# Performance work log

Hardware: AMD Instinct MI355X
Metric: run time of the kernel (lower is better)

## Reference

```python
import jax, jax.numpy as jnp
import numpy as np

NUM_CLASSES = 20   # M = len(unique(true)); label 0 is background (skipped)
ALPHA = 0.7
BETA = 1.5


def setup_inputs() -> dict:
    key = jax.random.key(0)
    k1, k2, k3 = jax.random.split(key, 3)
    B, N, K = 1, 262144, 128
    points = jax.random.normal(k1, (B, N, 3), dtype=jnp.float32)
    true = jax.random.randint(k2, (B, N), 0, NUM_CLASSES)
    embedding = jax.random.normal(k3, (B, N, K), dtype=jnp.float32)
    return {"points": points, "true": true, "embedding": embedding}


def reference(points, true, embedding):
    # points: (B,N,3), true: (B,N) int labels in [0,M), embedding: (B,N,K). B == 1.
    B, N, K = embedding.shape
    M = NUM_CLASSES
    t = true[0]  # (N,)

    # g = sigmoid(||p||) per point
    g = jax.nn.sigmoid(jnp.sqrt(jnp.sum(points ** 2, axis=-1)))  # (B,N)

    # per-cluster counts and embedding means (segment reduce over N)
    counts = jax.ops.segment_sum(jnp.ones((N,), points.dtype), t, num_segments=M)  # (M,)
    safe_counts = jnp.maximum(counts, 1.0)
    means = jax.ops.segment_sum(embedding[0], t, num_segments=M) / safe_counts[:, None]  # (M,K)

    # intra-cluster: per point, distance to its cluster mean
    d = jnp.sqrt(jnp.sum((embedding - means[true]) ** 2, axis=-1))  # (B,N)
    per_point = g * jnp.square(jnp.maximum(d - ALPHA, 0.0))         # (B,N)
    intra_per_cluster = jax.ops.segment_sum(per_point[0], t, num_segments=M) / safe_counts  # (M,)
    intra = jnp.sum(intra_per_cluster[1:])  # sum over clusters 1..M-1 (skip background 0)

    # inter-cluster: pairwise mean distances among foreground clusters
    me = means[1:]                                    # (M-1, K)
    sq = jnp.sum((me[:, None, :] - me[None, :, :]) ** 2, axis=-1)  # (M-1, M-1)
    eye = jnp.eye(M - 1, dtype=sq.dtype)
    dist = jnp.sqrt(jnp.where(eye > 0, 1.0, sq))      # safe sqrt on diagonal
    inter = jnp.sum((1.0 - eye) * jnp.square(jnp.maximum(BETA - dist, 0.0)))

    return jnp.broadcast_to(intra / M + inter / (M * (M - 1)), (B,))
```

## Files before the change

### kernel.cpp

```cpp
#include <hip/hip_runtime.h>
#include <hip/hip_bf16.h>
#include <math.h>

#define NCLS 20
#define KDIM 128
#define ALPHA 0.7f
#define BETA 1.5f

#define WS_SUMS 0
#define WS_INTRA 2560
#define WS_CUR 2580
#define WS_ZERO_N 2600
#define WS_G 4096

#define GRID 2048
#define SUMS_GRID 1027

__global__ void k_init(float* ws) {
    const int tid = threadIdx.x;
    for (int i = tid; i < WS_ZERO_N; i += 256) ws[i] = 0.0f;
}

__global__ void __launch_bounds__(256) k_scatter(const int* __restrict__ t,
                                                 const float* __restrict__ pts,
                                                 float* __restrict__ ws,
                                                 float* __restrict__ g,
                                                 int* __restrict__ bkt, int N) {
    __shared__ int ih[NCLS], lbase[NCLS];
    const int tid = threadIdx.x;
    if (tid < NCLS) ih[tid] = 0;
    __syncthreads();
    const int gid = blockIdx.x * 256 + tid;
    int c = -1, r = 0;
    if (gid < N) {
        c = t[gid];
        r = atomicAdd(&ih[c], 1);
        const float px = pts[(size_t)gid * 3 + 0];
        const float py = pts[(size_t)gid * 3 + 1];
        const float pz = pts[(size_t)gid * 3 + 2];
        const float rad = sqrtf(px * px + py * py + pz * pz);
        g[gid] = 1.0f / (1.0f + expf(-rad));
    }
    __syncthreads();
    if (tid < NCLS && ih[tid]) lbase[tid] = atomicAdd((int*)&ws[WS_CUR] + tid, ih[tid]);
    __syncthreads();
    if (c >= 0) bkt[(size_t)c * N + lbase[c] + r] = gid;
}

__device__ inline void hw_map(const int* gc, int u, int& cls, int& off, int& m) {
    cls = -1; off = 0; m = 0;
    int cum = 0;
#pragma unroll
    for (int c = 0; c < NCLS; c++) {
        const int cnt = gc[c];
        const int v = (cnt + 31) >> 5;
        if (u >= cum && u < cum + v) {
            cls = c;
            off = (u - cum) * 32;
            m = min(32, cnt - off);
        }
        cum += v;
    }
}

__global__ void __launch_bounds__(256) k_sums(const float4* __restrict__ emb4,
                                              const int* __restrict__ bkt,
                                              float* __restrict__ ws, int N) {
    __shared__ float lsum[NCLS * KDIM];
    const int tid = threadIdx.x;
    for (int i = tid; i < NCLS * KDIM; i += 256) lsum[i] = 0.0f;
    __syncthreads();

    const int s = tid & 31;
    const int u = blockIdx.x * 8 + (tid >> 5);
    int cls, off, m;
    hw_map((const int*)&ws[WS_CUR], u, cls, off, m);

    if (cls >= 0) {
        const int* b = bkt + (size_t)cls * N + off;
        const int bidx = b[min(s, m - 1)];
        float4 acc = make_float4(0.f, 0.f, 0.f, 0.f);
        if (m == 32) {
#pragma unroll
            for (int j0 = 0; j0 < 32; j0 += 8) {
                float4 v0, v1, v2, v3, v4, v5, v6, v7;
#define G(jj) { const int idx = __shfl(bidx, j0 + jj, 32);  \
                v##jj = emb4[(size_t)idx * 32 + s]; }
                G(0) G(1) G(2) G(3) G(4) G(5) G(6) G(7)
#undef G
                acc.x += v0.x + v1.x + v2.x + v3.x + v4.x + v5.x + v6.x + v7.x;
                acc.y += v0.y + v1.y + v2.y + v3.y + v4.y + v5.y + v6.y + v7.y;
                acc.z += v0.z + v1.z + v2.z + v3.z + v4.z + v5.z + v6.z + v7.z;
                acc.w += v0.w + v1.w + v2.w + v3.w + v4.w + v5.w + v6.w + v7.w;
            }
        } else {
            for (int j = 0; j < m; j++) {
                const int idx = __shfl(bidx, j, 32);
                const float4 v = emb4[(size_t)idx * 32 + s];
                acc.x += v.x; acc.y += v.y; acc.z += v.z; acc.w += v.w;
            }
        }
        float* a = &lsum[cls * KDIM + 4 * s];
        unsafeAtomicAdd(a + 0, acc.x);
        unsafeAtomicAdd(a + 1, acc.y);
        unsafeAtomicAdd(a + 2, acc.z);
        unsafeAtomicAdd(a + 3, acc.w);
    }
    __syncthreads();

    for (int i = tid; i < NCLS * KDIM; i += 256)
        if (lsum[i] != 0.0f) unsafeAtomicAdd(&ws[WS_SUMS + i], lsum[i]);
}

__global__ void __launch_bounds__(256) k_intra(const float4* __restrict__ emb4,
                                               const float* __restrict__ g,
                                               const int* __restrict__ bkt,
                                               float* __restrict__ ws, int N) {
    __shared__ float lmean[NCLS * KDIM];
    __shared__ float lintra[NCLS];
    const int tid = threadIdx.x;
    const int* gc = (const int*)&ws[WS_CUR];
    for (int i = tid; i < NCLS * KDIM; i += 256)
        lmean[i] = ws[WS_SUMS + i] / fmaxf((float)gc[i / KDIM], 1.0f);
    if (tid < NCLS) lintra[tid] = 0.0f;
    __syncthreads();

    const int s = tid & 31;
    const int u = blockIdx.x * 8 + (tid >> 5);
    int cls, off, m;
    hw_map(gc, u, cls, off, m);

    if (cls >= 0) {
        const float4 mr = *(const float4*)&lmean[cls * KDIM + 4 * s];
        const int* b = bkt + (size_t)cls * N + off;
        const int bidx = b[min(s, m - 1)];
        float part = 0.f;
        if (m == 32) {
#pragma unroll
            for (int j0 = 0; j0 < 32; j0 += 8) {
                float4 v0, v1, v2, v3, v4, v5, v6, v7;
                int i0, i1, i2, i3, i4, i5, i6, i7;
#define G(jj) { i##jj = __shfl(bidx, j0 + jj, 32);          \
                v##jj = emb4[(size_t)i##jj * 32 + s]; }
                G(0) G(1) G(2) G(3) G(4) G(5) G(6) G(7)
#undef G
#define P(jj) {                                                           \
    float dx = v##jj.x - mr.x, dy = v##jj.y - mr.y;                       \
    float dz = v##jj.z - mr.z, dw = v##jj.w - mr.w;                       \
    float d2 = dx * dx + dy * dy + dz * dz + dw * dw;                     \
    for (int o = 16; o >= 1; o >>= 1) d2 += __shfl_down(d2, o, 32);       \
    if (s == 0) {                                                         \
        const float d = sqrtf(d2);                                        \
        const float h = fmaxf(d - ALPHA, 0.0f);                           \
        part = fmaf(g[i##jj], h * h, part);                               \
    }                                                                     \
}
                P(0) P(1) P(2) P(3) P(4) P(5) P(6) P(7)
#undef P
            }
        } else {
            for (int j = 0; j < m; j++) {
                const int idx = __shfl(bidx, j, 32);
                const float4 v = emb4[(size_t)idx * 32 + s];
                float dx = v.x - mr.x, dy = v.y - mr.y;
                float dz = v.z - mr.z, dw = v.w - mr.w;
                float d2 = dx * dx + dy * dy + dz * dz + dw * dw;
                for (int o = 16; o >= 1; o >>= 1) d2 += __shfl_down(d2, o, 32);
                if (s == 0) {
                    const float d = sqrtf(d2);
                    const float h = fmaxf(d - ALPHA, 0.0f);
                    part = fmaf(g[idx], h * h, part);
                }
            }
        }
        if (s == 0 && part != 0.0f) unsafeAtomicAdd(&lintra[cls], part);
    }
    __syncthreads();
    if (tid < NCLS) unsafeAtomicAdd(&ws[WS_INTRA + tid], lintra[tid]);
}

__global__ void __launch_bounds__(256) k_final(const float* __restrict__ ws,
                                               float* __restrict__ out) {
    __shared__ float lmean[NCLS * KDIM];
    __shared__ float red[256];
    const int tid = threadIdx.x;
    const int* gc = (const int*)&ws[WS_CUR];
    for (int i = tid; i < NCLS * KDIM; i += 256)
        lmean[i] = ws[WS_SUMS + i] / fmaxf((float)gc[i / KDIM], 1.0f);
    __syncthreads();

    float acc = 0.0f;
    for (int idx = tid; idx < 361; idx += 256) {
        const int i = idx / 19 + 1;
        const int j = idx % 19 + 1;
        if (i != j) {
            float sq = 0.0f;
            const float* mi = lmean + i * KDIM;
            const float* mj = lmean + j * KDIM;
            for (int k = 0; k < KDIM; k++) {
                const float df = mi[k] - mj[k];
                sq += df * df;
            }
            const float dist = sqrtf(sq);
            const float h = fmaxf(BETA - dist, 0.0f);
            acc += h * h;
        }
    }
    red[tid] = acc;
    __syncthreads();
    for (int st = 128; st >= 1; st >>= 1) {
        if (tid < st) red[tid] += red[tid + st];
        __syncthreads();
    }
    if (tid == 0) {
        float intra = 0.0f;
        for (int c = 1; c < NCLS; c++)
            intra += ws[WS_INTRA + c] / fmaxf((float)gc[c], 1.0f);
        out[0] = intra / (float)NCLS + red[0] / (float)(NCLS * (NCLS - 1));
    }
}

#define FB_BLK 128
#define FB_GRID 2048
#define FBW_SUMS 0
#define FBW_CNT 2560
#define FBW_INTRA 2580
__global__ void __launch_bounds__(256) k_init_fb(float* ws) {
    const int tid = threadIdx.x;
    for (int i = tid; i < 2600; i += 256) ws[i] = 0.0f;
}
__global__ void __launch_bounds__(FB_BLK) k_sums_fb(const float4* __restrict__ emb4,
                                                    const int* __restrict__ t,
                                                    float* ws, int N) {
    __shared__ float lsum[2][NCLS * KDIM];
    __shared__ float lcnt[NCLS];
    __shared__ int lds_t[FB_BLK];
    const int tid = threadIdx.x;
    const int w = tid >> 6, k = tid & 63;
    const int half = k >> 5;
    const int k31 = k & 31;
    for (int i = tid; i < 2 * NCLS * KDIM; i += FB_BLK) (&lsum[0][0])[i] = 0.0f;
    if (tid < NCLS) lcnt[tid] = 0.0f;
    __syncthreads();
    const int chunk = blockIdx.x * FB_BLK;
    const int npts = min(FB_BLK, N - chunk);
    if (tid < npts) {
        const int c = t[chunk + tid];
        lds_t[tid] = c;
        unsafeAtomicAdd(&lcnt[c], 1.0f);
    }
    __syncthreads();
    float* L = lsum[w];
    for (int q = 32 * w; q < 32 * w + 32; q++) {
        const int pl = 2 * q + half;
        if (pl < npts) {
            const int c = lds_t[pl];
            const float4 v = emb4[(size_t)(chunk + pl) * 32 + k31];
            const int cA = __shfl(c, 0, 64);
            const int cB = __shfl(c, 32, 64);
            if (cA == cB) {
                float4 vv;
                vv.x = v.x + __shfl_xor(v.x, 32, 64);
                vv.y = v.y + __shfl_xor(v.y, 32, 64);
                vv.z = v.z + __shfl_xor(v.z, 32, 64);
                vv.w = v.w + __shfl_xor(v.w, 32, 64);
                if (half == 0) {
                    float4* a = (float4*)&L[cA * KDIM + 4 * k31];
                    float4 o = *a;
                    o.x += vv.x; o.y += vv.y; o.z += vv.z; o.w += vv.w;
                    *a = o;
                }
            } else {
                float4* a = (float4*)&L[c * KDIM + 4 * k31];
                float4 o = *a;
                o.x += v.x; o.y += v.y; o.z += v.z; o.w += v.w;
                *a = o;
            }
        }
    }
    __syncthreads();
    for (int i = tid; i < NCLS * KDIM; i += FB_BLK)
        unsafeAtomicAdd(&ws[FBW_SUMS + i], lsum[0][i] + lsum[1][i]);
    if (tid < NCLS) unsafeAtomicAdd(&ws[FBW_CNT + tid], lcnt[tid]);
}
__global__ void __launch_bounds__(256) k_intra_fb(const float4* __restrict__ emb4,
                                                  const int* __restrict__ t,
                                                  const float* __restrict__ pts,
                                                  float* ws, int N) {
    __shared__ float lmean[NCLS * KDIM];
    __shared__ float lintra[NCLS];
    const int tid = threadIdx.x;
    for (int i = tid; i < NCLS * KDIM; i += 256)
        lmean[i] = ws[FBW_SUMS + i] / fmaxf(ws[FBW_CNT + i / KDIM], 1.0f);
    if (tid < NCLS) lintra[tid] = 0.0f;
    __syncthreads();
    const int s = tid & 31;
    const int pp = tid >> 5;
    const int stride = FB_GRID * 8;
    for (int p = blockIdx.x * 8 + pp; p < N; p += stride) {
        const int c = t[p];
        const float4 v = emb4[(size_t)p * 32 + s];
        const float4 mm = *(const float4*)&lmean[c * KDIM + 4 * s];
        float dx = v.x - mm.x, dy = v.y - mm.y, dz = v.z - mm.z, dw = v.w - mm.w;
        float d2 = dx * dx + dy * dy + dz * dz + dw * dw;
        for (int off = 16; off >= 1; off >>= 1) d2 += __shfl_down(d2, off, 32);
        if (s == 0) {
            const float d = sqrtf(d2);
            const float px = pts[(size_t)p * 3 + 0];
            const float py = pts[(size_t)p * 3 + 1];
            const float pz = pts[(size_t)p * 3 + 2];
            const float r = sqrtf(px * px + py * py + pz * pz);
            const float gg = 1.0f / (1.0f + expf(-r));
            const float h = fmaxf(d - ALPHA, 0.0f);
            unsafeAtomicAdd(&lintra[c], gg * h * h);
        }
    }
    __syncthreads();
    if (tid < NCLS) unsafeAtomicAdd(&ws[FBW_INTRA + tid], lintra[tid]);
}
__global__ void __launch_bounds__(256) k_final_fb(const float* ws, float* out) {
    __shared__ float lmean[NCLS * KDIM];
    __shared__ float red[256];
    const int tid = threadIdx.x;
    for (int i = tid; i < NCLS * KDIM; i += 256)
        lmean[i] = ws[FBW_SUMS + i] / fmaxf(ws[FBW_CNT + i / KDIM], 1.0f);
    __syncthreads();
    float acc = 0.0f;
    for (int idx = tid; idx < 361; idx += 256) {
        const int i = idx / 19 + 1;
        const int j = idx % 19 + 1;
        if (i != j) {
            float sq = 0.0f;
            const float* mi = lmean + i * KDIM;
            const float* mj = lmean + j * KDIM;
            for (int k = 0; k < KDIM; k++) {
                const float df = mi[k] - mj[k];
                sq += df * df;
            }
            const float dist = sqrtf(sq);
            const float h = fmaxf(BETA - dist, 0.0f);
            acc += h * h;
        }
    }
    red[tid] = acc;
    __syncthreads();
    for (int st = 128; st >= 1; st >>= 1) {
        if (tid < st) red[tid] += red[tid + st];
        __syncthreads();
    }
    if (tid == 0) {
        float intra = 0.0f;
        for (int c = 1; c < NCLS; c++)
            intra += ws[FBW_INTRA + c] / fmaxf(ws[FBW_CNT + c], 1.0f);
        out[0] = intra / (float)NCLS + red[0] / (float)(NCLS * (NCLS - 1));
    }
}

extern "C" void kernel_launch(void* const* d_in, const int* in_sizes, int n_in,
                              void* d_out, int out_size, void* d_ws, size_t ws_size,
                              hipStream_t stream) {
    const float* pts = (const float*)d_in[0];
    const int* t = (const int*)d_in[1];
    const float4* emb4 = (const float4*)d_in[2];
    float* out = (float*)d_out;
    float* ws = (float*)d_ws;
    const int N = in_sizes[1];
    float* g = ws + WS_G;
    int* bkt = (int*)(g + N);
    const size_t need = ((size_t)WS_G + (size_t)N + (size_t)NCLS * (size_t)N) * 4;

    if (ws_size >= need) {
        k_init<<<1, 256, 0, stream>>>(ws);
        k_scatter<<<(N + 255) / 256, 256, 0, stream>>>(t, pts, ws, g, bkt, N);
        k_sums<<<SUMS_GRID, 256, 0, stream>>>(emb4, bkt, ws, N);
        k_intra<<<SUMS_GRID, 256, 0, stream>>>(emb4, g, bkt, ws, N);
        k_final<<<1, 256, 0, stream>>>(ws, out);
    } else {
        k_init_fb<<<1, 256, 0, stream>>>(ws);
        k_sums_fb<<<FB_GRID, FB_BLK, 0, stream>>>(emb4, t, ws, N);
        k_intra_fb<<<FB_GRID, 256, 0, stream>>>(emb4, t, pts, ws, N);
        k_final_fb<<<1, 256, 0, stream>>>(ws, out);
    }
}
```

Measured before the change: 114.9 us.

## Stage class-sorted bf16 embedding copy in k_sums and read it in k_intra

k_sums now also writes a bf16 copy of each gathered embedding row into a class-contiguous scratch buffer, along with a sorted copy of g. k_intra then reads these sequentially, at half the bytes, instead of re-gathering fp32 rows through the bucket indices. The aim is to cut the second pass's memory traffic and replace scattered reads with streaming ones. The cost is extra write traffic in k_sums (64 MB of embeddings becomes 32 MB written plus 32 MB read), a larger workspace requirement that could push execution onto the fallback path, and bf16 rounding error in the distances.

```diff
diff --git a/kernel.cpp b/kernel.cpp
--- a/kernel.cpp
+++ b/kernel.cpp
@@ -13,8 +13,12 @@
 #define WS_ZERO_N 2600
 #define WS_G 4096
 
-#define GRID 2048
 #define SUMS_GRID 1027
+
+__device__ __forceinline__ unsigned short f2bf(float f) {
+    const unsigned u = __float_as_uint(f);
+    return (unsigned short)((u + 0x8000u) >> 16);
+}
 
 __global__ void k_init(float* ws) {
     const int tid = threadIdx.x;
@@ -47,9 +51,10 @@
     if (c >= 0) bkt[(size_t)c * N + lbase[c] + r] = gid;
 }
 
-__device__ inline void hw_map(const int* gc, int u, int& cls, int& off, int& m) {
-    cls = -1; off = 0; m = 0;
-    int cum = 0;
+__device__ inline void hw_map(const int* gc, int u, int& cls, int& off, int& m,
+                              int& pstart) {
+    cls = -1; off = 0; m = 0; pstart = 0;
+    int cum = 0, pfx = 0;
 #pragma unroll
     for (int c = 0; c < NCLS; c++) {
         const int cnt = gc[c];
@@ -58,13 +63,18 @@
             cls = c;
             off = (u - cum) * 32;
             m = min(32, cnt - off);
+            pstart = pfx;
         }
         cum += v;
+        pfx += cnt;
     }
 }
 
 __global__ void __launch_bounds__(256) k_sums(const float4* __restrict__ emb4,
                                               const int* __restrict__ bkt,
+                                              const float* __restrict__ g,
+                                              float* __restrict__ gs,
+                                              unsigned short* __restrict__ sb,
                                               float* __restrict__ ws, int N) {
     __shared__ float lsum[NCLS * KDIM];
     const int tid = threadIdx.x;
@@ -73,13 +83,23 @@
 
     const int s = tid & 31;
     const int u = blockIdx.x * 8 + (tid >> 5);
-    int cls, off, m;
-    hw_map((const int*)&ws[WS_CUR], u, cls, off, m);
+    int cls, off, m, pstart;
+    hw_map((const int*)&ws[WS_CUR], u, cls, off, m, pstart);
 
     if (cls >= 0) {
         const int* b = bkt + (size_t)cls * N + off;
         const int bidx = b[min(s, m - 1)];
+        if (s < m) gs[pstart + off + s] = g[bidx];
         float4 acc = make_float4(0.f, 0.f, 0.f, 0.f);
+
+#define WSB(jj, J0)                                                           \
+        {                                                                     \
+            const size_t pos = (size_t)(pstart + off + (J0) + (jj));          \
+            ushort4 o;                                                        \
+            o.x = f2bf(v##jj.x); o.y = f2bf(v##jj.y);                         \
+            o.z = f2bf(v##jj.z); o.w = f2bf(v##jj.w);                         \
+            *(ushort4*)(sb + pos * 128 + 4 * s) = o;                          \
+        }
         if (m == 32) {
 #pragma unroll
             for (int j0 = 0; j0 < 32; j0 += 8) {
@@ -92,14 +112,18 @@
                 acc.y += v0.y + v1.y + v2.y + v3.y + v4.y + v5.y + v6.y + v7.y;
                 acc.z += v0.z + v1.z + v2.z + v3.z + v4.z + v5.z + v6.z + v7.z;
                 acc.w += v0.w + v1.w + v2.w + v3.w + v4.w + v5.w + v6.w + v7.w;
+                WSB(0, j0) WSB(1, j0) WSB(2, j0) WSB(3, j0)
+                WSB(4, j0) WSB(5, j0) WSB(6, j0) WSB(7, j0)
             }
         } else {
             for (int j = 0; j < m; j++) {
                 const int idx = __shfl(bidx, j, 32);
-                const float4 v = emb4[(size_t)idx * 32 + s];
-                acc.x += v.x; acc.y += v.y; acc.z += v.z; acc.w += v.w;
-            }
-        }
+                const float4 v0 = emb4[(size_t)idx * 32 + s];
+                acc.x += v0.x; acc.y += v0.y; acc.z += v0.z; acc.w += v0.w;
+                WSB(0, j)
+            }
+        }
+#undef WSB
         float* a = &lsum[cls * KDIM + 4 * s];
         unsafeAtomicAdd(a + 0, acc.x);
         unsafeAtomicAdd(a + 1, acc.y);
@@ -112,9 +136,8 @@
         if (lsum[i] != 0.0f) unsafeAtomicAdd(&ws[WS_SUMS + i], lsum[i]);
 }
 
-__global__ void __launch_bounds__(256) k_intra(const float4* __restrict__ emb4,
-                                               const float* __restrict__ g,
-                                               const int* __restrict__ bkt,
+__global__ void __launch_bounds__(256) k_intra(const unsigned short* __restrict__ sb,
+                                               const float* __restrict__ gs,
                                                float* __restrict__ ws, int N) {
     __shared__ float lmean[NCLS * KDIM];
     __shared__ float lintra[NCLS];
@@ -126,54 +149,63 @@
     __syncthreads();
 
     const int s = tid & 31;
+    const int sl = s & 15;
+    const int h = s >> 4;
     const int u = blockIdx.x * 8 + (tid >> 5);
-    int cls, off, m;
-    hw_map(gc, u, cls, off, m);
+    int cls, off, m, pstart;
+    hw_map(gc, u, cls, off, m, pstart);
 
     if (cls >= 0) {
-        const float4 mr = *(const float4*)&lmean[cls * KDIM + 4 * s];
-        const int* b = bkt + (size_t)cls * N + off;
-        const int bidx = b[min(s, m - 1)];
-        float part = 0.f;
+        const float4 ma = *(const float4*)&lmean[cls * KDIM + 8 * sl];
+        const float4 mb = *(const float4*)&lmean[cls * KDIM + 8 * sl + 4];
+        const size_t base = (size_t)(pstart + off);
+        float part = 0.0f;
+
+#define PPOINT(PJ, VALID)                                                     \
+        {                                                                     \
+            const size_t pos = base + (PJ);                                   \
+            const uint4 raw = *(const uint4*)(sb + pos * 128 + 8 * sl);       \
+            float d2 = 0.f;                                                   \
+            {                                                                 \
+                const float f0 = __uint_as_float((raw.x & 0xffffu) << 16);    \
+                const float f1 = __uint_as_float(raw.x & 0xffff0000u);        \
+                const float f2 = __uint_as_float((raw.y & 0xffffu) << 16);    \
+                const float f3 = __uint_as_float(raw.y & 0xffff0000u);        \
+                const float f4 = __uint_as_float((raw.z & 0xffffu) << 16);    \
+                const float f5 = __uint_as_float(raw.z & 0xffff0000u);        \
+                const float f6 = __uint_as_float((raw.w & 0xffffu) << 16);    \
+                const float f7 = __uint_as_float(raw.w & 0xffff0000u);        \
+                const float e0 = f0 - ma.x, e1 = f1 - ma.y;                   \
+                const float e2 = f2 - ma.z, e3 = f3 - ma.w;                   \
+                const float e4 = f4 - mb.x, e5 = f5 - mb.y;                   \
+                const float e6 = f6 - mb.z, e7 = f7 - mb.w;                   \
+                d2 = e0 * e0 + e1 * e1 + e2 * e2 + e3 * e3 +                  \
+                     e4 * e4 + e5 * e5 + e6 * e6 + e7 * e7;                   \
+            }                                                                 \
+            d2 += __shfl_down(d2, 8, 16);                                     \
+            d2 += __shfl_down(d2, 4, 16);                                     \
+            d2 += __shfl_down(d2, 2, 16);                                     \
+            d2 += __shfl_down(d2, 1, 16);                                     \
+            if (sl == 0 && (VALID)) {                                         \
+                const float d = sqrtf(d2);                                    \
+                const float hg = fmaxf(d - ALPHA, 0.0f);                      \
+                part = fmaf(gs[pos], hg * hg, part);                          \
+            }                                                                 \
+        }
+
         if (m == 32) {
 #pragma unroll
-            for (int j0 = 0; j0 < 32; j0 += 8) {
-                float4 v0, v1, v2, v3, v4, v5, v6, v7;
-                int i0, i1, i2, i3, i4, i5, i6, i7;
-#define G(jj) { i##jj = __shfl(bidx, j0 + jj, 32);          \
-                v##jj = emb4[(size_t)i##jj * 32 + s]; }
-                G(0) G(1) G(2) G(3) G(4) G(5) G(6) G(7)
-#undef G
-#define P(jj) {                                                           \
-    float dx = v##jj.x - mr.x, dy = v##jj.y - mr.y;                       \
-    float dz = v##jj.z - mr.z, dw = v##jj.w - mr.w;                       \
-    float d2 = dx * dx + dy * dy + dz * dz + dw * dw;                     \
-    for (int o = 16; o >= 1; o >>= 1) d2 += __shfl_down(d2, o, 32);       \
-    if (s == 0) {                                                         \
-        const float d = sqrtf(d2);                                        \
-        const float h = fmaxf(d - ALPHA, 0.0f);                           \
-        part = fmaf(g[i##jj], h * h, part);                               \
-    }                                                                     \
-}
-                P(0) P(1) P(2) P(3) P(4) P(5) P(6) P(7)
-#undef P
+            for (int j0 = 0; j0 < 32; j0 += 2) {
+                PPOINT(j0 + h, true)
             }
         } else {
-            for (int j = 0; j < m; j++) {
-                const int idx = __shfl(bidx, j, 32);
-                const float4 v = emb4[(size_t)idx * 32 + s];
-                float dx = v.x - mr.x, dy = v.y - mr.y;
-                float dz = v.z - mr.z, dw = v.w - mr.w;
-                float d2 = dx * dx + dy * dy + dz * dz + dw * dw;
-                for (int o = 16; o >= 1; o >>= 1) d2 += __shfl_down(d2, o, 32);
-                if (s == 0) {
-                    const float d = sqrtf(d2);
-                    const float h = fmaxf(d - ALPHA, 0.0f);
-                    part = fmaf(g[idx], h * h, part);
-                }
-            }
-        }
-        if (s == 0 && part != 0.0f) unsafeAtomicAdd(&lintra[cls], part);
+            for (int j0 = 0; j0 < m; j0 += 2) {
+                const int pj = j0 + h;
+                PPOINT(min(pj, m - 1), pj < m)
+            }
+        }
+#undef PPOINT
+        if (sl == 0 && part != 0.0f) unsafeAtomicAdd(&lintra[cls], part);
     }
     __syncthreads();
     if (tid < NCLS) unsafeAtomicAdd(&ws[WS_INTRA + tid], lintra[tid]);
@@ -202,8 +234,8 @@
                 sq += df * df;
             }
             const float dist = sqrtf(sq);
-            const float h = fmaxf(BETA - dist, 0.0f);
-            acc += h * h;
+            const float hh = fmaxf(BETA - dist, 0.0f);
+            acc += hh * hh;
         }
     }
     red[tid] = acc;
@@ -311,8 +343,8 @@
             const float pz = pts[(size_t)p * 3 + 2];
             const float r = sqrtf(px * px + py * py + pz * pz);
             const float gg = 1.0f / (1.0f + expf(-r));
-            const float h = fmaxf(d - ALPHA, 0.0f);
-            unsafeAtomicAdd(&lintra[c], gg * h * h);
+            const float hh = fmaxf(d - ALPHA, 0.0f);
+            unsafeAtomicAdd(&lintra[c], gg * hh * hh);
         }
     }
     __syncthreads();
@@ -338,8 +370,8 @@
                 sq += df * df;
             }
             const float dist = sqrtf(sq);
-            const float h = fmaxf(BETA - dist, 0.0f);
-            acc += h * h;
+            const float hh = fmaxf(BETA - dist, 0.0f);
+            acc += hh * hh;
         }
     }
     red[tid] = acc;
@@ -365,15 +397,19 @@
     float* out = (float*)d_out;
     float* ws = (float*)d_ws;
     const int N = in_sizes[1];
+
     float* g = ws + WS_G;
-    int* bkt = (int*)(g + N);
-    const size_t need = ((size_t)WS_G + (size_t)N + (size_t)NCLS * (size_t)N) * 4;
+    float* gs = g + N;
+    int* bkt = (int*)(gs + N);
+    unsigned short* sb = (unsigned short*)(bkt + (size_t)NCLS * N);
+    const size_t need = ((size_t)WS_G + 2 * (size_t)N + (size_t)NCLS * N) * 4 +
+                        (size_t)N * KDIM * 2;
 
     if (ws_size >= need) {
         k_init<<<1, 256, 0, stream>>>(ws);
         k_scatter<<<(N + 255) / 256, 256, 0, stream>>>(t, pts, ws, g, bkt, N);
-        k_sums<<<SUMS_GRID, 256, 0, stream>>>(emb4, bkt, ws, N);
-        k_intra<<<SUMS_GRID, 256, 0, stream>>>(emb4, g, bkt, ws, N);
+        k_sums<<<SUMS_GRID, 256, 0, stream>>>(emb4, bkt, g, gs, sb, ws, N);
+        k_intra<<<SUMS_GRID, 256, 0, stream>>>(sb, gs, ws, N);
         k_final<<<1, 256, 0, stream>>>(ws, out);
     } else {
         k_init_fb<<<1, 256, 0, stream>>>(ws);
```

After: 111.8 us. -2.7%, faster.
